# Performance work log

Hardware: AMD Instinct MI355X
Metric: run time of the kernel (lower is better)

The kernel has to match this reference:

```python
import jax, jax.numpy as jnp
import numpy as np

B, T, C, H = 8, 1024, 1024, 16
D = C // H  # head dim = 64

def setup_inputs() -> dict:
    key = jax.random.key(0)
    k1, k2, k3 = jax.random.split(key, 3)
    x = jax.random.normal(k1, (B, T, C), dtype=jnp.float32)
    W_attn = jax.random.normal(k2, (C, 3 * C), dtype=jnp.float32) * (1.0 / np.sqrt(C))
    W_proj = jax.random.normal(k3, (C, C), dtype=jnp.float32) * (1.0 / np.sqrt(C))
    # Llama RoPE frequencies: base^(-2i/D)
    omega = (10000.0 ** (-jnp.arange(0, D, 2, dtype=jnp.float32) / D))  # [D/2]
    return {"x": x, "W_attn": W_attn, "W_proj": W_proj, "omega": omega}

def _apply_rope(x, omega):
    # x: [B, T, H, D]; omega: [D/2]
    t = x.shape[1]
    ang = jnp.arange(t, dtype=x.dtype)[:, None] * omega[None, :]  # [T, D/2]
    cos = jnp.cos(ang)[None, :, None, :]  # [1, T, 1, D/2]
    sin = jnp.sin(ang)[None, :, None, :]
    d2 = x.shape[-1] // 2
    x1, x2 = x[..., :d2], x[..., d2:]
    return jnp.concatenate([x1 * cos - x2 * sin, x2 * cos + x1 * sin], axis=-1)

def reference(x, W_attn, W_proj, omega):
    b, t, c = x.shape
    qkv = jnp.einsum('btc,cd->btd', x, W_attn)  # fused QKV projection
    q, k, v = jnp.split(qkv, 3, axis=-1)
    q = q.reshape(b, t, H, D)
    k = k.reshape(b, t, H, D)
    v = v.reshape(b, t, H, D)
    q = _apply_rope(q, omega)
    k = _apply_rope(k, omega)
    # non-causal SDPA
    scale = 1.0 / jnp.sqrt(jnp.asarray(D, dtype=x.dtype))
    scores = jnp.einsum('bqhd,bkhd->bhqk', q, k) * scale
    probs = jax.nn.softmax(scores, axis=-1)
    y = jnp.einsum('bhqk,bkhd->bqhd', probs, v).reshape(b, t, c)
    return jnp.einsum('btc,cd->btd', y, W_proj)
```

## Files before the change

### kernel.cpp

```cpp
#include <hip/hip_runtime.h>
#include <hip/hip_bf16.h>
#include <stdint.h>


typedef __attribute__((ext_vector_type(8))) short short8;
typedef __attribute__((ext_vector_type(4))) float floatx4;
typedef __attribute__((ext_vector_type(2))) unsigned int uint2v;

#define DEV static __device__ __forceinline__

#if __has_builtin(__builtin_amdgcn_exp2f)
#define EXP2(x) __builtin_amdgcn_exp2f(x)
#else
#define EXP2(x) exp2f(x)
#endif

DEV uint16_t f2bf(float f) {
  union { float f; uint32_t i; } v; v.f = f;
  uint32_t u = v.i;
  return (uint16_t)((u + 0x7fffu + ((u >> 16) & 1u)) >> 16);
}

DEV uint32_t pkbf(float a, float b) {
  __hip_bfloat162 h = __float22bfloat162_rn(make_float2(a, b));
  union { __hip_bfloat162 h; uint32_t u; } v; v.h = h;
  return v.u;
}

DEV void async_load16(const uint16_t* g, uint16_t* l) {
  __builtin_amdgcn_global_load_lds(
      (const __attribute__((address_space(1))) void*)g,
      (__attribute__((address_space(3))) void*)l, 16, 0, 0);
}

__global__ __launch_bounds__(256) void prep(
    const float* __restrict__ x, const float* __restrict__ W_attn,
    const float* __restrict__ W_proj, const float* __restrict__ omega,
    uint16_t* __restrict__ xb, uint16_t* __restrict__ Wt_attn,
    uint16_t* __restrict__ Wt_proj, float2* __restrict__ tab) {
  __shared__ uint16_t tile[64][65];
  const int blk = blockIdx.x, tid = threadIdx.x;
  if (blk < 4096) {
    const size_t base = ((size_t)blk * 256 + tid) * 8;
    floatx4 a = *(const floatx4*)(x + base);
    floatx4 b = *(const floatx4*)(x + base + 4);
    short8 s;
    s[0] = (short)f2bf(a[0]); s[1] = (short)f2bf(a[1]);
    s[2] = (short)f2bf(a[2]); s[3] = (short)f2bf(a[3]);
    s[4] = (short)f2bf(b[0]); s[5] = (short)f2bf(b[1]);
    s[6] = (short)f2bf(b[2]); s[7] = (short)f2bf(b[3]);
    *(short8*)(xb + base) = s;
  } else if (blk < 5120) {
    const float* in;
    uint16_t* out;
    int R = 1024, Ccols, bx, by;
    if (blk < 4864) {
      const int idx = blk - 4096;
      in = W_attn; out = Wt_attn; Ccols = 3072;
      bx = idx % 48; by = idx / 48;
    } else {
      const int idx = blk - 4864;
      in = W_proj; out = Wt_proj; Ccols = 1024;
      bx = idx % 16; by = idx / 16;
    }
    const int tx = tid & 63, ty = tid >> 6;
    const int c0 = bx * 64, r0 = by * 64;
    #pragma unroll
    for (int i = 0; i < 64; i += 4)
      tile[ty + i][tx] = f2bf(in[(size_t)(r0 + ty + i) * Ccols + c0 + tx]);
    __syncthreads();
    #pragma unroll
    for (int i = 0; i < 64; i += 4)
      out[(size_t)(c0 + ty + i) * R + r0 + tx] = tile[tx][ty + i];
  } else {
    const int idx = (blk - 5120) * 256 + tid;
    const int t = idx >> 5, d = idx & 31;
    float s, c;
    sincosf((float)t * omega[d], &s, &c);
    tab[idx] = make_float2(c, s);
  }
}

DEV void gemm_core8(const uint16_t* __restrict__ Ag,
                    const uint16_t* __restrict__ Bg,
                    int row0, int col0,
                    uint16_t* As, uint16_t* Bs, floatx4 (&acc)[4][4]) {
  const int tid = threadIdx.x;
  const int wave = tid >> 6, lane = tid & 63;
  const int l15 = lane & 15, quad = lane >> 4;
  const int wrow = wave >> 1, wcol = wave & 1;
  const int sw = l15 & 7;
  const int K = 1024;

  size_t aoff[4], boff[2];
  #pragma unroll
  for (int i = 0; i < 4; i++) {
    const int e = i * 512 + tid;
    const int r = e >> 3, c = e & 7, j = c ^ (r & 7);
    aoff[i] = (size_t)(row0 + r) * K + j * 8;
  }
  #pragma unroll
  for (int i = 0; i < 2; i++) {
    const int e = i * 512 + tid;
    const int r = e >> 3, c = e & 7, j = c ^ (r & 7);
    boff[i] = (size_t)(col0 + r) * K + j * 8;
  }

  #pragma unroll
  for (int t = 0; t < 2; t++) {
    #pragma unroll
    for (int i = 0; i < 2; i++)
      async_load16(Bg + boff[i] + (size_t)t * 64, Bs + t * 8192 + (i * 512 + tid) * 8);
    #pragma unroll
    for (int i = 0; i < 4; i++)
      async_load16(Ag + aoff[i] + (size_t)t * 64, As + t * 16384 + (i * 512 + tid) * 8);
  }

  const floatx4 z4 = {0.f, 0.f, 0.f, 0.f};
  #pragma unroll
  for (int mi = 0; mi < 4; mi++)
    #pragma unroll
    for (int ni = 0; ni < 4; ni++) acc[mi][ni] = z4;

  asm volatile("s_waitcnt vmcnt(6)" ::: "memory");
  __builtin_amdgcn_s_barrier();

  int qa = 0, q2 = 2;
  const int arow = wrow * 64 + l15;
  const int brow = wcol * 64 + l15;
  for (int kt = 0; kt < 16; ++kt) {
    const uint16_t* Aq = As + qa * 16384;
    const uint16_t* Bq = Bs + qa * 8192;
    uint16_t* As2 = As + q2 * 16384;
    uint16_t* Bs2 = Bs + q2 * 8192;
    const size_t k2 = (size_t)(kt + 2) * 64;

    short8 af[4], bfr[4];
    #pragma unroll
    for (int mi = 0; mi < 4; mi++)
      af[mi] = *(const short8*)(Aq + (arow + mi * 16) * 64 + ((quad ^ sw) * 8));
    #pragma unroll
    for (int ni = 0; ni < 4; ni++)
      bfr[ni] = *(const short8*)(Bq + (brow + ni * 16) * 64 + ((quad ^ sw) * 8));
    if (kt < 14) {
      #pragma unroll
      for (int i = 0; i < 2; i++)
        async_load16(Bg + boff[i] + k2, Bs2 + (i * 512 + tid) * 8);
      #pragma unroll
      for (int i = 0; i < 2; i++)
        async_load16(Ag + aoff[i] + k2, As2 + (i * 512 + tid) * 8);
    }
    __builtin_amdgcn_s_barrier();
    asm volatile("s_waitcnt lgkmcnt(0)" ::: "memory");
    __builtin_amdgcn_s_setprio(1);
    #pragma unroll
    for (int mi = 0; mi < 4; mi++)
      #pragma unroll
      for (int ni = 0; ni < 4; ni++)
        acc[mi][ni] = __builtin_amdgcn_mfma_f32_16x16x32_bf16(
            af[mi], bfr[ni], acc[mi][ni], 0, 0, 0);
    __builtin_amdgcn_s_setprio(0);
    __builtin_amdgcn_s_barrier();

    #pragma unroll
    for (int mi = 0; mi < 4; mi++)
      af[mi] = *(const short8*)(Aq + (arow + mi * 16) * 64 + (((4 + quad) ^ sw) * 8));
    #pragma unroll
    for (int ni = 0; ni < 4; ni++)
      bfr[ni] = *(const short8*)(Bq + (brow + ni * 16) * 64 + (((4 + quad) ^ sw) * 8));
    if (kt < 14) {
      #pragma unroll
      for (int i = 2; i < 4; i++)
        async_load16(Ag + aoff[i] + k2, As2 + (i * 512 + tid) * 8);
      asm volatile("s_waitcnt vmcnt(6)" ::: "memory");
    } else if (kt == 14) {
      asm volatile("s_waitcnt vmcnt(0)" ::: "memory");
    }
    __builtin_amdgcn_s_barrier();
    asm volatile("s_waitcnt lgkmcnt(0)" ::: "memory");
    __builtin_amdgcn_s_setprio(1);
    #pragma unroll
    for (int mi = 0; mi < 4; mi++)
      #pragma unroll
      for (int ni = 0; ni < 4; ni++)
        acc[mi][ni] = __builtin_amdgcn_mfma_f32_16x16x32_bf16(
            af[mi], bfr[ni], acc[mi][ni], 0, 0, 0);
    __builtin_amdgcn_s_setprio(0);
    __builtin_amdgcn_s_barrier();

    qa = (qa == 2) ? 0 : qa + 1;
    q2 = (q2 == 2) ? 0 : q2 + 1;
  }
}

__global__ __launch_bounds__(512) void gemm_qkv(
    const uint16_t* __restrict__ A, const uint16_t* __restrict__ Bt,
    const float2* __restrict__ tab,
    uint16_t* __restrict__ Qr, uint16_t* __restrict__ Kr, uint16_t* __restrict__ Vt) {
  __shared__ __align__(16) uint16_t As[3 * 256 * 64];
  __shared__ __align__(16) uint16_t Bs[3 * 128 * 64];
  const int bid = blockIdx.x;
  const int xcd = bid & 7, slot = bid >> 3;
  const int row0 = (xcd * 4 + (slot & 3)) * 256;
  const int col0 = (slot >> 2) * 128;
  floatx4 acc[4][4];
  gemm_core8(A, Bt, row0, col0, As, Bs, acc);

  const int tid = threadIdx.x;
  const int wave = tid >> 6, lane = tid & 63;
  const int l15 = lane & 15, quad = lane >> 4;
  const int cblk = col0 + (wave & 1) * 64;
  const int region = cblk >> 10;
  const int h = (cblk & 1023) >> 6;
  const int rr = row0 + (wave >> 1) * 64;
  const int b = rr >> 10;
  const int tbase = rr & 1023;
  const size_t bh = (size_t)b * 16 + h;

  if (region < 2) {
    uint16_t* dst = (region == 0) ? Qr : Kr;
    const float scl = (region == 0) ? 0.125f * 1.44269504088896f : 1.0f;
    #pragma unroll
    for (int mi = 0; mi < 4; mi++)
      #pragma unroll
      for (int r = 0; r < 4; r++) {
        const int t = tbase + mi * 16 + quad * 4 + r;
        const size_t base = (bh * 1024 + t) * 64;
        const float2 cs0 = tab[t * 32 + l15];
        const float2 cs1 = tab[t * 32 + l15 + 16];
        {
          float x1 = acc[mi][0][r], x2 = acc[mi][2][r];
          dst[base + l15]      = f2bf((x1 * cs0.x - x2 * cs0.y) * scl);
          dst[base + l15 + 32] = f2bf((x2 * cs0.x + x1 * cs0.y) * scl);
        }
        {
          float x1 = acc[mi][1][r], x2 = acc[mi][3][r];
          dst[base + 16 + l15]      = f2bf((x1 * cs1.x - x2 * cs1.y) * scl);
          dst[base + 16 + l15 + 32] = f2bf((x2 * cs1.x + x1 * cs1.y) * scl);
        }
      }
  } else {
    #pragma unroll
    for (int mi = 0; mi < 4; mi++)
      #pragma unroll
      for (int ni = 0; ni < 4; ni++) {
        const int d = ni * 16 + l15;
        #pragma unroll
        for (int r = 0; r < 4; r++) {
          const int t = tbase + mi * 16 + quad * 4 + r;
          Vt[bh * 65536 + (size_t)d * 1024 + t] = f2bf(acc[mi][ni][r]);
        }
      }
  }
}

__global__ __launch_bounds__(512) void gemm_out(
    const uint16_t* __restrict__ A, const uint16_t* __restrict__ Bt,
    float* __restrict__ Cmat, int M, int N, int K) {
  __shared__ __align__(16) uint16_t As[3 * 256 * 64];
  __shared__ __align__(16) uint16_t Bs[3 * 128 * 64];
  const int bid = blockIdx.x;
  const int xcd = bid & 7, slot = bid >> 3;
  const int row0 = (xcd * 4 + (slot & 3)) * 256;
  const int col0 = (slot >> 2) * 128;
  floatx4 acc[4][4];
  gemm_core8(A, Bt, row0, col0, As, Bs, acc);

  const int tid = threadIdx.x;
  const int wave = tid >> 6, lane = tid & 63;
  const int l15 = lane & 15, quad = lane >> 4;
  #pragma unroll
  for (int mi = 0; mi < 4; mi++)
    #pragma unroll
    for (int ni = 0; ni < 4; ni++) {
      const int col = col0 + (wave & 1) * 64 + ni * 16 + l15;
      #pragma unroll
      for (int r = 0; r < 4; r++) {
        const int row = row0 + (wave >> 1) * 64 + mi * 16 + quad * 4 + r;
        Cmat[(size_t)row * N + col] = acc[mi][ni][r];
      }
    }
}

#define FLD 72

__global__ __launch_bounds__(512) void flash_attn(
    const uint16_t* __restrict__ Qr, const uint16_t* __restrict__ Kr,
    const uint16_t* __restrict__ Vt, uint16_t* __restrict__ Y) {
  __shared__ __align__(16) uint16_t Ks[2][64 * 64];
  __shared__ __align__(16) uint16_t Vs[2][64 * 64];
  __shared__ __align__(16) uint16_t Ps[512 * FLD];
  const int tid = threadIdx.x;
  const int wv = tid >> 6, lane = tid & 63;
  const int l15 = lane & 15, quad = lane >> 4;
  const int sw = l15 & 7;
  const int bh = blockIdx.x & 127, qt = blockIdx.x >> 7;
  const int b = bh >> 4, h = bh & 15;
  const int q0 = qt * 512;
  const uint16_t* Qbh = Qr + (size_t)bh * 65536;
  const uint16_t* Kbh = Kr + (size_t)bh * 65536;
  const uint16_t* Vbh = Vt + (size_t)bh * 65536;

  short8 bq[4][2];
  #pragma unroll
  for (int g = 0; g < 4; g++)
    #pragma unroll
    for (int ks = 0; ks < 2; ks++)
      bq[g][ks] = *(const short8*)(Qbh +
          (size_t)(q0 + wv * 64 + g * 16 + l15) * 64 + ks * 32 + quad * 8);

  float psum[4] = {0.f, 0.f, 0.f, 0.f};
  const floatx4 z4 = {0.f, 0.f, 0.f, 0.f};
  floatx4 oacc[4][4];
  #pragma unroll
  for (int g = 0; g < 4; g++)
    #pragma unroll
    for (int mi = 0; mi < 4; mi++) oacc[g][mi] = z4;

  #define STAGE_KV(kt_, Kd_, Vd_)                                               \
    {                                                                           \
      const int e = tid;                                                        \
      const int r = e >> 3;                                                     \
      const int j = (e & 7) ^ (r & 7);                                          \
      async_load16(Kbh + (size_t)((kt_) * 64 + r) * 64 + j * 8, (Kd_) + e * 8); \
      async_load16(Vbh + (size_t)r * 1024 + (kt_) * 64 + j * 8, (Vd_) + e * 8); \
    }

  STAGE_KV(0, Ks[0], Vs[0]);
  STAGE_KV(1, Ks[1], Vs[1]);
  asm volatile("s_waitcnt vmcnt(2)" ::: "memory");
  __builtin_amdgcn_s_barrier();

  for (int kt = 0; kt < 16; kt++) {
    const int buf = kt & 1;
    #pragma unroll
    for (int g = 0; g < 4; g++) {
      const int qrow = wv * 64 + g * 16 + l15;
      floatx4 sacc[4];
      __builtin_amdgcn_s_setprio(1);
      #pragma unroll
      for (int ni = 0; ni < 4; ni++) {
        sacc[ni] = z4;
        #pragma unroll
        for (int ks = 0; ks < 2; ks++) {
          short8 ak = *(const short8*)(&Ks[buf][(ni * 16 + l15) * 64 +
                                               (((ks * 4 + quad) ^ sw) * 8)]);
          sacc[ni] = __builtin_amdgcn_mfma_f32_16x16x32_bf16(ak, bq[g][ks], sacc[ni], 0, 0, 0);
        }
      }
      __builtin_amdgcn_s_setprio(0);
      #pragma unroll
      for (int ni = 0; ni < 4; ni++) {
        float p0 = EXP2(sacc[ni][0]), p1 = EXP2(sacc[ni][1]);
        float p2 = EXP2(sacc[ni][2]), p3 = EXP2(sacc[ni][3]);
        psum[g] += (p0 + p1) + (p2 + p3);
        uint2v pk; pk[0] = pkbf(p0, p1); pk[1] = pkbf(p2, p3);
        *(uint2v*)(&Ps[qrow * FLD + ni * 16 + quad * 4]) = pk;
      }
      short8 bp[2];
      #pragma unroll
      for (int ks = 0; ks < 2; ks++)
        bp[ks] = *(const short8*)(&Ps[qrow * FLD + ks * 32 + quad * 8]);
      __builtin_amdgcn_s_setprio(1);
      #pragma unroll
      for (int mi = 0; mi < 4; mi++) {
        #pragma unroll
        for (int ks = 0; ks < 2; ks++) {
          short8 av = *(const short8*)(&Vs[buf][(mi * 16 + l15) * 64 +
                                               (((ks * 4 + quad) ^ sw) * 8)]);
          oacc[g][mi] = __builtin_amdgcn_mfma_f32_16x16x32_bf16(av, bp[ks], oacc[g][mi], 0, 0, 0);
        }
      }
      __builtin_amdgcn_s_setprio(0);
    }
    __builtin_amdgcn_s_barrier();
    if (kt + 2 < 16) { STAGE_KV(kt + 2, Ks[buf], Vs[buf]); }
    if (kt + 1 < 16) {
      if (kt + 2 < 16) asm volatile("s_waitcnt vmcnt(2)" ::: "memory");
      else             asm volatile("s_waitcnt vmcnt(0)" ::: "memory");
      __builtin_amdgcn_s_barrier();
    }
  }
  #undef STAGE_KV

  #pragma unroll
  for (int g = 0; g < 4; g++) {
    float l_tot = psum[g];
    l_tot += __shfl_xor(l_tot, 16, 64);
    l_tot += __shfl_xor(l_tot, 32, 64);
    const float linv = 1.0f / l_tot;
    const int t = q0 + wv * 64 + g * 16 + l15;
    #pragma unroll
    for (int mi = 0; mi < 4; mi++) {
      uint2v yk;
      yk[0] = pkbf(oacc[g][mi][0] * linv, oacc[g][mi][1] * linv);
      yk[1] = pkbf(oacc[g][mi][2] * linv, oacc[g][mi][3] * linv);
      *(uint2v*)(Y + (size_t)(b * 1024 + t) * 1024 + h * 64 + mi * 16 + quad * 4) = yk;
    }
  }
}

extern "C" void kernel_launch(void* const* d_in, const int* in_sizes, int n_in,
                              void* d_out, int out_size, void* d_ws, size_t ws_size,
                              hipStream_t stream) {
  const float* x      = (const float*)d_in[0];
  const float* W_attn = (const float*)d_in[1];
  const float* W_proj = (const float*)d_in[2];
  const float* omega  = (const float*)d_in[3];
  float* out = (float*)d_out;

  uint16_t* wsp     = (uint16_t*)d_ws;
  uint16_t* xb      = wsp;
  uint16_t* Wt_attn = xb + (size_t)8192 * 1024;
  uint16_t* Wt_proj = Wt_attn + (size_t)3072 * 1024;
  uint16_t* Qr      = Wt_proj + (size_t)1024 * 1024;
  uint16_t* Kr      = Qr + (size_t)128 * 1024 * 64;
  uint16_t* Vt      = Kr + (size_t)128 * 1024 * 64;
  float2*   ropet   = (float2*)(Vt + (size_t)128 * 1024 * 64);
  uint16_t* Y       = xb;

  prep<<<5248, 256, 0, stream>>>(x, W_attn, W_proj, omega, xb, Wt_attn, Wt_proj, ropet);
  gemm_qkv<<<768, 512, 0, stream>>>(xb, Wt_attn, ropet, Qr, Kr, Vt);
  flash_attn<<<256, 512, 0, stream>>>(Qr, Kr, Vt, Y);
  gemm_out<<<256, 512, 0, stream>>>(Y, Wt_proj, out, 8192, 1024, 1024);
}
```

Baseline: 233.0 us.

## Enlarge QKV GEMM tile to 256x256 with K-step 32 and 2x4 waves

The QKV projection kernel gets its own inlined GEMM loop with a 256x256 output tile per block instead of 256x128. Each wave now computes 128x64 using 8x4 accumulators, and K is stepped by 32 with a 3-stage LDS ring and a new XOR swizzle. This halves the grid to 384 blocks and raises arithmetic intensity per LDS and global load. In exchange it doubles accumulator register pressure, which may lower occupancy, and it leaves fewer blocks to fill the CUs.

```diff
diff --git a/kernel.cpp b/kernel.cpp
--- a/kernel.cpp
+++ b/kernel.cpp
@@ -81,138 +81,116 @@
   }
 }
 
-DEV void gemm_core8(const uint16_t* __restrict__ Ag,
-                    const uint16_t* __restrict__ Bg,
-                    int row0, int col0,
-                    uint16_t* As, uint16_t* Bs, floatx4 (&acc)[4][4]) {
-  const int tid = threadIdx.x;
-  const int wave = tid >> 6, lane = tid & 63;
-  const int l15 = lane & 15, quad = lane >> 4;
-  const int wrow = wave >> 1, wcol = wave & 1;
-  const int sw = l15 & 7;
-  const int K = 1024;
-
-  size_t aoff[4], boff[2];
-  #pragma unroll
-  for (int i = 0; i < 4; i++) {
-    const int e = i * 512 + tid;
-    const int r = e >> 3, c = e & 7, j = c ^ (r & 7);
-    aoff[i] = (size_t)(row0 + r) * K + j * 8;
-  }
-  #pragma unroll
-  for (int i = 0; i < 2; i++) {
-    const int e = i * 512 + tid;
-    const int r = e >> 3, c = e & 7, j = c ^ (r & 7);
-    boff[i] = (size_t)(col0 + r) * K + j * 8;
-  }
-
-  #pragma unroll
-  for (int t = 0; t < 2; t++) {
-    #pragma unroll
-    for (int i = 0; i < 2; i++)
-      async_load16(Bg + boff[i] + (size_t)t * 64, Bs + t * 8192 + (i * 512 + tid) * 8);
-    #pragma unroll
-    for (int i = 0; i < 4; i++)
-      async_load16(Ag + aoff[i] + (size_t)t * 64, As + t * 16384 + (i * 512 + tid) * 8);
-  }
-
-  const floatx4 z4 = {0.f, 0.f, 0.f, 0.f};
-  #pragma unroll
-  for (int mi = 0; mi < 4; mi++)
-    #pragma unroll
-    for (int ni = 0; ni < 4; ni++) acc[mi][ni] = z4;
-
-  asm volatile("s_waitcnt vmcnt(6)" ::: "memory");
-  __builtin_amdgcn_s_barrier();
-
-  int qa = 0, q2 = 2;
-  const int arow = wrow * 64 + l15;
-  const int brow = wcol * 64 + l15;
-  for (int kt = 0; kt < 16; ++kt) {
-    const uint16_t* Aq = As + qa * 16384;
-    const uint16_t* Bq = Bs + qa * 8192;
-    uint16_t* As2 = As + q2 * 16384;
-    uint16_t* Bs2 = Bs + q2 * 8192;
-    const size_t k2 = (size_t)(kt + 2) * 64;
-
-    short8 af[4], bfr[4];
-    #pragma unroll
-    for (int mi = 0; mi < 4; mi++)
-      af[mi] = *(const short8*)(Aq + (arow + mi * 16) * 64 + ((quad ^ sw) * 8));
-    #pragma unroll
-    for (int ni = 0; ni < 4; ni++)
-      bfr[ni] = *(const short8*)(Bq + (brow + ni * 16) * 64 + ((quad ^ sw) * 8));
-    if (kt < 14) {
-      #pragma unroll
-      for (int i = 0; i < 2; i++)
-        async_load16(Bg + boff[i] + k2, Bs2 + (i * 512 + tid) * 8);
-      #pragma unroll
-      for (int i = 0; i < 2; i++)
-        async_load16(Ag + aoff[i] + k2, As2 + (i * 512 + tid) * 8);
-    }
-    __builtin_amdgcn_s_barrier();
-    asm volatile("s_waitcnt lgkmcnt(0)" ::: "memory");
-    __builtin_amdgcn_s_setprio(1);
-    #pragma unroll
-    for (int mi = 0; mi < 4; mi++)
-      #pragma unroll
-      for (int ni = 0; ni < 4; ni++)
-        acc[mi][ni] = __builtin_amdgcn_mfma_f32_16x16x32_bf16(
-            af[mi], bfr[ni], acc[mi][ni], 0, 0, 0);
-    __builtin_amdgcn_s_setprio(0);
-    __builtin_amdgcn_s_barrier();
-
-    #pragma unroll
-    for (int mi = 0; mi < 4; mi++)
-      af[mi] = *(const short8*)(Aq + (arow + mi * 16) * 64 + (((4 + quad) ^ sw) * 8));
-    #pragma unroll
-    for (int ni = 0; ni < 4; ni++)
-      bfr[ni] = *(const short8*)(Bq + (brow + ni * 16) * 64 + (((4 + quad) ^ sw) * 8));
-    if (kt < 14) {
-      #pragma unroll
-      for (int i = 2; i < 4; i++)
-        async_load16(Ag + aoff[i] + k2, As2 + (i * 512 + tid) * 8);
-      asm volatile("s_waitcnt vmcnt(6)" ::: "memory");
-    } else if (kt == 14) {
-      asm volatile("s_waitcnt vmcnt(0)" ::: "memory");
-    }
-    __builtin_amdgcn_s_barrier();
-    asm volatile("s_waitcnt lgkmcnt(0)" ::: "memory");
-    __builtin_amdgcn_s_setprio(1);
-    #pragma unroll
-    for (int mi = 0; mi < 4; mi++)
-      #pragma unroll
-      for (int ni = 0; ni < 4; ni++)
-        acc[mi][ni] = __builtin_amdgcn_mfma_f32_16x16x32_bf16(
-            af[mi], bfr[ni], acc[mi][ni], 0, 0, 0);
-    __builtin_amdgcn_s_setprio(0);
-    __builtin_amdgcn_s_barrier();
-
-    qa = (qa == 2) ? 0 : qa + 1;
-    q2 = (q2 == 2) ? 0 : q2 + 1;
-  }
-}
-
 __global__ __launch_bounds__(512) void gemm_qkv(
     const uint16_t* __restrict__ A, const uint16_t* __restrict__ Bt,
     const float2* __restrict__ tab,
     uint16_t* __restrict__ Qr, uint16_t* __restrict__ Kr, uint16_t* __restrict__ Vt) {
-  __shared__ __align__(16) uint16_t As[3 * 256 * 64];
-  __shared__ __align__(16) uint16_t Bs[3 * 128 * 64];
+  __shared__ __align__(16) uint16_t As[3 * 256 * 32];
+  __shared__ __align__(16) uint16_t Bs[3 * 256 * 32];
+  const int tid = threadIdx.x;
+  const int wave = tid >> 6, lane = tid & 63;
+  const int l15 = lane & 15, quad = lane >> 4;
+  const int wrow = wave >> 2, wcol = wave & 3;
+  const int sw2 = (l15 >> 1) & 3;
+  const int K = 1024;
+
   const int bid = blockIdx.x;
   const int xcd = bid & 7, slot = bid >> 3;
   const int row0 = (xcd * 4 + (slot & 3)) * 256;
-  const int col0 = (slot >> 2) * 128;
-  floatx4 acc[4][4];
-  gemm_core8(A, Bt, row0, col0, As, Bs, acc);
-
-  const int tid = threadIdx.x;
-  const int wave = tid >> 6, lane = tid & 63;
-  const int l15 = lane & 15, quad = lane >> 4;
-  const int cblk = col0 + (wave & 1) * 64;
+  const int col0 = (slot >> 2) * 256;
+
+  size_t aoff[2], boff[2];
+  #pragma unroll
+  for (int i = 0; i < 2; i++) {
+    const int e = i * 512 + tid;
+    const int r = e >> 2, c = e & 3;
+    const int j = c ^ ((r >> 1) & 3);
+    aoff[i] = (size_t)(row0 + r) * K + j * 8;
+    boff[i] = (size_t)(col0 + r) * K + j * 8;
+  }
+  #pragma unroll
+  for (int t = 0; t < 2; t++)
+    #pragma unroll
+    for (int i = 0; i < 2; i++) {
+      async_load16(A + aoff[i] + (size_t)t * 32, As + t * 8192 + (i * 512 + tid) * 8);
+      async_load16(Bt + boff[i] + (size_t)t * 32, Bs + t * 8192 + (i * 512 + tid) * 8);
+    }
+
+  floatx4 acc[8][4];
+  const floatx4 z4 = {0.f, 0.f, 0.f, 0.f};
+  #pragma unroll
+  for (int mi = 0; mi < 8; mi++)
+    #pragma unroll
+    for (int ni = 0; ni < 4; ni++) acc[mi][ni] = z4;
+
+  asm volatile("s_waitcnt vmcnt(4)" ::: "memory");
+  __builtin_amdgcn_s_barrier();
+
+  int qa = 0, q2 = 2;
+  const int arow = wrow * 128 + l15;
+  const int brow = wcol * 64 + l15;
+  for (int kt = 0; kt < 32; ++kt) {
+    const uint16_t* Aq = As + qa * 8192;
+    const uint16_t* Bq = Bs + qa * 8192;
+    uint16_t* As2 = As + q2 * 8192;
+    uint16_t* Bs2 = Bs + q2 * 8192;
+    const size_t k2 = (size_t)(kt + 2) * 32;
+
+    short8 af[4], bfr[4];
+    #pragma unroll
+    for (int ni = 0; ni < 4; ni++)
+      bfr[ni] = *(const short8*)(Bq + (brow + ni * 16) * 32 + ((quad ^ sw2) * 8));
+    #pragma unroll
+    for (int m = 0; m < 4; m++)
+      af[m] = *(const short8*)(Aq + (arow + m * 16) * 32 + ((quad ^ sw2) * 8));
+    if (kt < 30) {
+      #pragma unroll
+      for (int i = 0; i < 2; i++)
+        async_load16(A + aoff[i] + k2, As2 + (i * 512 + tid) * 8);
+    }
+    __builtin_amdgcn_s_barrier();
+    asm volatile("s_waitcnt lgkmcnt(0)" ::: "memory");
+    __builtin_amdgcn_s_setprio(1);
+    #pragma unroll
+    for (int m = 0; m < 4; m++)
+      #pragma unroll
+      for (int ni = 0; ni < 4; ni++)
+        acc[m][ni] = __builtin_amdgcn_mfma_f32_16x16x32_bf16(
+            af[m], bfr[ni], acc[m][ni], 0, 0, 0);
+    __builtin_amdgcn_s_setprio(0);
+    __builtin_amdgcn_s_barrier();
+
+    #pragma unroll
+    for (int m = 0; m < 4; m++)
+      af[m] = *(const short8*)(Aq + (arow + (m + 4) * 16) * 32 + ((quad ^ sw2) * 8));
+    if (kt < 30) {
+      #pragma unroll
+      for (int i = 0; i < 2; i++)
+        async_load16(Bt + boff[i] + k2, Bs2 + (i * 512 + tid) * 8);
+      asm volatile("s_waitcnt vmcnt(4)" ::: "memory");
+    } else if (kt == 30) {
+      asm volatile("s_waitcnt vmcnt(0)" ::: "memory");
+    }
+    __builtin_amdgcn_s_barrier();
+    asm volatile("s_waitcnt lgkmcnt(0)" ::: "memory");
+    __builtin_amdgcn_s_setprio(1);
+    #pragma unroll
+    for (int m = 0; m < 4; m++)
+      #pragma unroll
+      for (int ni = 0; ni < 4; ni++)
+        acc[m + 4][ni] = __builtin_amdgcn_mfma_f32_16x16x32_bf16(
+            af[m], bfr[ni], acc[m + 4][ni], 0, 0, 0);
+    __builtin_amdgcn_s_setprio(0);
+    __builtin_amdgcn_s_barrier();
+
+    qa = (qa == 2) ? 0 : qa + 1;
+    q2 = (q2 == 2) ? 0 : q2 + 1;
+  }
+
+  const int cblk = col0 + wcol * 64;
   const int region = cblk >> 10;
   const int h = (cblk & 1023) >> 6;
-  const int rr = row0 + (wave >> 1) * 64;
+  const int rr = row0 + wrow * 128;
   const int b = rr >> 10;
   const int tbase = rr & 1023;
   const size_t bh = (size_t)b * 16 + h;
@@ -221,7 +199,7 @@
     uint16_t* dst = (region == 0) ? Qr : Kr;
     const float scl = (region == 0) ? 0.125f * 1.44269504088896f : 1.0f;
     #pragma unroll
-    for (int mi = 0; mi < 4; mi++)
+    for (int mi = 0; mi < 8; mi++)
       #pragma unroll
       for (int r = 0; r < 4; r++) {
         const int t = tbase + mi * 16 + quad * 4 + r;
@@ -241,7 +219,7 @@
       }
   } else {
     #pragma unroll
-    for (int mi = 0; mi < 4; mi++)
+    for (int mi = 0; mi < 8; mi++)
       #pragma unroll
       for (int ni = 0; ni < 4; ni++) {
         const int d = ni * 16 + l15;
@@ -251,6 +229,118 @@
           Vt[bh * 65536 + (size_t)d * 1024 + t] = f2bf(acc[mi][ni][r]);
         }
       }
+  }
+}
+
+DEV void gemm_core8(const uint16_t* __restrict__ Ag,
+                    const uint16_t* __restrict__ Bg,
+                    int row0, int col0,
+                    uint16_t* As, uint16_t* Bs, floatx4 (&acc)[4][4]) {
+  const int tid = threadIdx.x;
+  const int wave = tid >> 6, lane = tid & 63;
+  const int l15 = lane & 15, quad = lane >> 4;
+  const int wrow = wave >> 1, wcol = wave & 1;
+  const int sw = l15 & 7;
+  const int K = 1024;
+
+  size_t aoff[4], boff[2];
+  #pragma unroll
+  for (int i = 0; i < 4; i++) {
+    const int e = i * 512 + tid;
+    const int r = e >> 3, c = e & 7, j = c ^ (r & 7);
+    aoff[i] = (size_t)(row0 + r) * K + j * 8;
+  }
+  #pragma unroll
+  for (int i = 0; i < 2; i++) {
+    const int e = i * 512 + tid;
+    const int r = e >> 3, c = e & 7, j = c ^ (r & 7);
+    boff[i] = (size_t)(col0 + r) * K + j * 8;
+  }
+
+  #pragma unroll
+  for (int t = 0; t < 2; t++) {
+    #pragma unroll
+    for (int i = 0; i < 2; i++)
+      async_load16(Bg + boff[i] + (size_t)t * 64, Bs + t * 8192 + (i * 512 + tid) * 8);
+    #pragma unroll
+    for (int i = 0; i < 4; i++)
+      async_load16(Ag + aoff[i] + (size_t)t * 64, As + t * 16384 + (i * 512 + tid) * 8);
+  }
+
+  const floatx4 z4 = {0.f, 0.f, 0.f, 0.f};
+  #pragma unroll
+  for (int mi = 0; mi < 4; mi++)
+    #pragma unroll
+    for (int ni = 0; ni < 4; ni++) acc[mi][ni] = z4;
+
+  asm volatile("s_waitcnt vmcnt(6)" ::: "memory");
+  __builtin_amdgcn_s_barrier();
+
+  int qa = 0, q2 = 2;
+  const int arow = wrow * 64 + l15;
+  const int brow = wcol * 64 + l15;
+  for (int kt = 0; kt < 16; ++kt) {
+    const uint16_t* Aq = As + qa * 16384;
+    const uint16_t* Bq = Bs + qa * 8192;
+    uint16_t* As2 = As + q2 * 16384;
+    uint16_t* Bs2 = Bs + q2 * 8192;
+    const size_t k2 = (size_t)(kt + 2) * 64;
+
+    short8 af[4], bfr[4];
+    #pragma unroll
+    for (int mi = 0; mi < 4; mi++)
+      af[mi] = *(const short8*)(Aq + (arow + mi * 16) * 64 + ((quad ^ sw) * 8));
+    #pragma unroll
+    for (int ni = 0; ni < 4; ni++)
+      bfr[ni] = *(const short8*)(Bq + (brow + ni * 16) * 64 + ((quad ^ sw) * 8));
+    if (kt < 14) {
+      #pragma unroll
+      for (int i = 0; i < 2; i++)
+        async_load16(Bg + boff[i] + k2, Bs2 + (i * 512 + tid) * 8);
+      #pragma unroll
+      for (int i = 0; i < 2; i++)
+        async_load16(Ag + aoff[i] + k2, As2 + (i * 512 + tid) * 8);
+    }
+    __builtin_amdgcn_s_barrier();
+    asm volatile("s_waitcnt lgkmcnt(0)" ::: "memory");
+    __builtin_amdgcn_s_setprio(1);
+    #pragma unroll
+    for (int mi = 0; mi < 4; mi++)
+      #pragma unroll
+      for (int ni = 0; ni < 4; ni++)
+        acc[mi][ni] = __builtin_amdgcn_mfma_f32_16x16x32_bf16(
+            af[mi], bfr[ni], acc[mi][ni], 0, 0, 0);
+    __builtin_amdgcn_s_setprio(0);
+    __builtin_amdgcn_s_barrier();
+
+    #pragma unroll
+    for (int mi = 0; mi < 4; mi++)
+      af[mi] = *(const short8*)(Aq + (arow + mi * 16) * 64 + (((4 + quad) ^ sw) * 8));
+    #pragma unroll
+    for (int ni = 0; ni < 4; ni++)
+      bfr[ni] = *(const short8*)(Bq + (brow + ni * 16) * 64 + (((4 + quad) ^ sw) * 8));
+    if (kt < 14) {
+      #pragma unroll
+      for (int i = 2; i < 4; i++)
+        async_load16(Ag + aoff[i] + k2, As2 + (i * 512 + tid) * 8);
+      asm volatile("s_waitcnt vmcnt(6)" ::: "memory");
+    } else if (kt == 14) {
+      asm volatile("s_waitcnt vmcnt(0)" ::: "memory");
+    }
+    __builtin_amdgcn_s_barrier();
+    asm volatile("s_waitcnt lgkmcnt(0)" ::: "memory");
+    __builtin_amdgcn_s_setprio(1);
+    #pragma unroll
+    for (int mi = 0; mi < 4; mi++)
+      #pragma unroll
+      for (int ni = 0; ni < 4; ni++)
+        acc[mi][ni] = __builtin_amdgcn_mfma_f32_16x16x32_bf16(
+            af[mi], bfr[ni], acc[mi][ni], 0, 0, 0);
+    __builtin_amdgcn_s_setprio(0);
+    __builtin_amdgcn_s_barrier();
+
+    qa = (qa == 2) ? 0 : qa + 1;
+    q2 = (q2 == 2) ? 0 : q2 + 1;
   }
 }
 
@@ -420,7 +510,7 @@
   uint16_t* Y       = xb;
 
   prep<<<5248, 256, 0, stream>>>(x, W_attn, W_proj, omega, xb, Wt_attn, Wt_proj, ropet);
-  gemm_qkv<<<768, 512, 0, stream>>>(xb, Wt_attn, ropet, Qr, Kr, Vt);
+  gemm_qkv<<<384, 512, 0, stream>>>(xb, Wt_attn, ropet, Qr, Kr, Vt);
   flash_attn<<<256, 512, 0, stream>>>(Qr, Kr, Vt, Y);
   gemm_out<<<256, 512, 0, stream>>>(Y, Wt_proj, out, 8192, 1024, 1024);
 }
```

Measured after the change: 243.8 us. +4.6%, slower.
